# Kernel optimization log

Hardware: AMD Instinct MI355X
Metric: run time of the kernel (lower is better)

## Reference

```python
import jax, jax.numpy as jnp
import numpy as np

HID = 256
NUM_LAYERS = 2


def setup_inputs() -> dict:
    key = jax.random.key(0)
    k0, k1, k2, k3 = jax.random.split(key, 4)
    B, R, C, I = 64, 32, 32, 8
    stdv = 1.0 / np.sqrt(HID)
    inp = jax.random.normal(k0, (B, R, C, I), jnp.float32)
    W_first = jax.random.uniform(k1, (6 * HID, I + 2 * HID), jnp.float32, -stdv, stdv)
    W_other = jax.random.uniform(k2, (NUM_LAYERS - 1, 6 * HID, 4 * HID), jnp.float32, -stdv, stdv)
    Bias = jax.random.uniform(k3, (NUM_LAYERS, 6 * HID), jnp.float32, -stdv, stdv)
    return {"input": inp, "W_first": W_first, "W_other": W_other, "Bias": Bias,
            "batch_size": B, "input_size": I, "flag": 0}


def _run_layer(a, W, b, H):
    # a: [R, B, L, F_in] diagonally-shifted input; W: [6H, F_in+2H]; b: [6H]
    R, Bb, L, _ = a.shape
    C = L - R + 1
    h0 = jnp.zeros((R, Bb, H), a.dtype)

    def step(carry, inputs):
        h_row, h_col = carry
        x_t, t = inputs
        z = jnp.concatenate([h_row, h_col, x_t], axis=-1)        # [R,B,2H+F]
        gate = jnp.einsum('rbf,gf->rbg', z, W)                   # [R,B,6H]
        # torch: bias added only to first B*(t+1) rows, and only when t < R
        mask = ((jnp.arange(R) <= t) & (t < R))[:, None, None]
        gate = jnp.where(mask, gate + b, gate)
        sig = jax.nn.sigmoid(gate[..., :4 * H])
        tnh = jnp.tanh(gate[..., 4 * H:])
        u_r, o_r, u_c, o_c = jnp.split(sig, 4, axis=-1)
        i_r, i_c = jnp.split(tnh, 2, axis=-1)
        h_row = jnp.tanh((1 - u_r) * h_row + u_r * i_r) * o_r
        h_col = jnp.tanh((1 - u_c) * h_col + u_c * i_c) * o_c
        out = jnp.concatenate([h_row, h_col], axis=-1)           # [R,B,2H]
        # row state that would be saved at this step (valid for t >= C-1)
        row_save = jax.lax.dynamic_index_in_dim(
            h_row, jnp.clip(t - (C - 1), 0, R - 1), axis=0, keepdims=False)
        col_save = h_col[R - 1]                                  # saved pre-roll
        h_col = jnp.roll(h_col, 1, axis=0)                       # roll by batch_size == shift slice axis by 1
        return (h_row, h_col), (out, row_save, col_save)

    xs = (jnp.moveaxis(a, 2, 0), jnp.arange(L))
    _, (outs, row_saves, col_saves) = jax.lax.scan(step, (h0, h0), xs)
    a_next = jnp.moveaxis(outs, 0, 2)        # [R, B, L, 2H]
    hidden_row = row_saves[C - 1:]           # [R, B, H]  (steps t >= C-1)
    hidden_col = col_saves[R - 1:]           # [C, B, H]  (steps t >= R-1)
    return a_next, hidden_row, hidden_col


def _forward(input, W_first, W_other, Bias, flag):
    H = Bias.shape[-1] // 6
    num_layers = Bias.shape[0]
    x = jnp.transpose(input, (2, 0, 1, 3)) if flag == 1 else jnp.transpose(input, (1, 0, 2, 3))
    R, Bb, C, I = x.shape
    L = R + C - 1
    # input_transfer[r, :, r:r+C, :] = x[r]  -> pad then roll each slice by r
    xp = jnp.pad(x, ((0, 0), (0, 0), (0, R - 1), (0, 0)))        # [R,B,L,I]
    a = jax.vmap(lambda xr, r: jnp.roll(xr, r, axis=1))(xp, jnp.arange(R))
    rows, cols = [], []
    for layer in range(num_layers):
        W = W_first if layer == 0 else W_other[layer - 1]
        a, hr, hc = _run_layer(a, W, Bias[layer], H)             # dropout=0 / eval: identity
        rows.append(hr)
        cols.append(hc)
    output_all = a.reshape(R * Bb, L, 2 * H)
    hidden_row_all = jnp.transpose(jnp.stack(rows), (2, 0, 1, 3))  # [B, NL, R, H]
    hidden_col_all = jnp.transpose(jnp.stack(cols), (2, 0, 1, 3))  # [B, NL, C, H]
    if flag == 1:
        return output_all, hidden_col_all, hidden_row_all
    return output_all, hidden_row_all, hidden_col_all


def reference(input, W_first, W_other, Bias, batch_size, input_size, flag):
    return _forward(input, W_first, W_other, Bias, flag)
```

## Files before the change

kernel.cpp:

```cpp
#include <hip/hip_runtime.h>

typedef __bf16 bf16x8 __attribute__((ext_vector_type(8)));
typedef float  f32x4  __attribute__((ext_vector_type(4)));

#define Z0S 520
#define Z1S 1032
#define W0P_ELEMS (2 * 8 * 17 * 6 * 512)
#define W1P_ELEMS (2 * 8 * 32 * 6 * 512)
#define XB_ELEMS (2 * 64 * 32 * 512)

__device__ __forceinline__ unsigned short f2bf(float f) {
    unsigned int u = __builtin_bit_cast(unsigned int, f);
    u += 0x7fffu + ((u >> 16) & 1u);
    return (unsigned short)(u >> 16);
}
__device__ __forceinline__ float sigm(float x) {
    x = fminf(30.f, fmaxf(-30.f, x));
    return __fdividef(1.0f, 1.0f + __expf(-x));
}
__device__ __forceinline__ float ftanh(float x) {
    x = fminf(15.f, fmaxf(-15.f, x));
    float e = __expf(2.0f * x);
    return 1.0f - __fdividef(2.0f, e + 1.0f);
}
__device__ __forceinline__ bf16x8 zero8() {
    bf16x8 v;
#pragma unroll
    for (int i = 0; i < 8; ++i) v[i] = (__bf16)0.0f;
    return v;
}
__device__ __forceinline__ void st_f32_wt(float* p, float v) {
    __hip_atomic_store(p, v, __ATOMIC_RELAXED, __HIP_MEMORY_SCOPE_AGENT);
}
__device__ __forceinline__ void st_u16_wt(unsigned short* p, unsigned short v) {
    __hip_atomic_store(p, v, __ATOMIC_RELAXED, __HIP_MEMORY_SCOPE_AGENT);
}

__global__ void convert_w(const float* __restrict__ W0f, const float* __restrict__ W1f,
                          unsigned short* __restrict__ W0p, unsigned short* __restrict__ W1p,
                          int* __restrict__ flags) {
    const int gid = blockIdx.x * blockDim.x + threadIdx.x;
    const int stride = gridDim.x * blockDim.x;
    if (gid < 512) flags[gid] = 0;
    for (int i = gid; i < W0P_ELEMS; i += stride) {
        const int e = i & 7, lane = (i >> 3) & 63;
        const int r = i >> 9;
        const int G = r % 6;  const int r2 = r / 6;
        const int ks = r2 % 17; const int gcg = r2 / 17;
        const int jj = gcg * 16 + (lane & 15);
        const int k = ks * 32 + (lane >> 4) * 8 + e;
        float v = 0.f;
        if (k < 520) v = W0f[(size_t)(G * 256 + jj) * 520 + k];
        W0p[i] = f2bf(v);
    }
    for (int i = gid; i < W1P_ELEMS; i += stride) {
        const int e = i & 7, lane = (i >> 3) & 63;
        const int r = i >> 9;
        const int G = r % 6;  const int r2 = r / 6;
        const int ks = r2 & 31; const int gcg = r2 >> 5;
        const int jj = gcg * 16 + (lane & 15);
        const int k = ks * 32 + (lane >> 4) * 8 + e;
        W1p[i] = f2bf(W1f[(size_t)(G * 256 + jj) * 1024 + k]);
    }
}

__global__ __launch_bounds__(512, 2) void witran_coop(
    const float* __restrict__ inp,
    const unsigned short* __restrict__ W0p,
    const unsigned short* __restrict__ W1p,
    const float* __restrict__ Bias,
    float* __restrict__ out,
    unsigned short* __restrict__ xb0,
    unsigned short* __restrict__ xb1,
    int* __restrict__ flags)
{
    const int bid  = blockIdx.x;
    const int r8   = bid & 7;
    const int s    = r8 >> 1;
    const int b    = (bid >> 3) * 2 + (r8 & 1);
    const int tid  = threadIdx.x;
    const int wave = tid >> 6;
    const int cg   = wave >> 1;
    const int gh   = wave & 1;
    const int lane = tid & 63;
    const int quad = lane >> 4;
    const int l16  = lane & 15;
    const int jl   = cg * 16 + l16;
    const int jj   = s * 64 + jl;
    const int gcg  = jj >> 4;
    const int Gs0 = 2 * gh, Gs1 = 2 * gh + 1, Gs2 = 4 + gh;

    int* f0 = flags;
    int* f1 = flags + 256;
    const int fown = b * 4 + s;

    __shared__ __align__(16) unsigned short z0[32 * Z0S];
    __shared__ __align__(16) unsigned short z1[32 * Z1S];
    __shared__ float rollbuf[32 * 64];

    for (int idx = tid; idx < 32 * Z0S; idx += 512) z0[idx] = 0;
    for (int idx = tid; idx < 32 * Z1S; idx += 512) z1[idx] = 0;
    __syncthreads();
    if (tid < 256) {
        const int m = tid >> 3, i = tid & 7;
        const int c = 0 - m;
        float v = 0.f;
        if (c >= 0 && c < 32) v = inp[((b * 32 + m) * 32 + c) * 8 + i];
        z0[m * Z0S + 512 + i] = f2bf(v);
    }

    float biasr[2][3];
#pragma unroll
    for (int L = 0; L < 2; ++L) {
        biasr[L][0] = Bias[L * 1536 + Gs0 * 256 + jj];
        biasr[L][1] = Bias[L * 1536 + Gs1 * 256 + jj];
        biasr[L][2] = Bias[L * 1536 + Gs2 * 256 + jj];
    }

    float streg[2][2][4];
#pragma unroll
    for (int L = 0; L < 2; ++L)
#pragma unroll
        for (int mh = 0; mh < 2; ++mh)
#pragma unroll
            for (int p = 0; p < 4; ++p) streg[L][mh][p] = 0.f;

    const unsigned short* w0g[3];
    const unsigned short* w1g[3];
    w0g[0] = W0p + (size_t)gcg * (17 * 6 * 512) + Gs0 * 512 + lane * 8;
    w0g[1] = W0p + (size_t)gcg * (17 * 6 * 512) + Gs1 * 512 + lane * 8;
    w0g[2] = W0p + (size_t)gcg * (17 * 6 * 512) + Gs2 * 512 + lane * 8;
    w1g[0] = W1p + (size_t)gcg * (32 * 6 * 512) + Gs0 * 512 + lane * 8;
    w1g[1] = W1p + (size_t)gcg * (32 * 6 * 512) + Gs1 * 512 + lane * 8;
    w1g[2] = W1p + (size_t)gcg * (32 * 6 * 512) + Gs2 * 512 + lane * 8;
    const unsigned short* aB0m[2] = { &z0[l16 * Z0S], &z0[(16 + l16) * Z0S] };
    const unsigned short* aB1m[2] = { &z1[l16 * Z1S], &z1[(16 + l16) * Z1S] };

    __syncthreads();

    const size_t OUT1 = 66060288u;
    const size_t OUT2 = OUT1 + 1048576u;

    const int sr   = tid >> 4;
    const int srem = tid & 15;
    const int sreg = srem >> 3;
    const int sc8  = (srem & 7) * 8;
    const int sr1  = (sr + 1) & 31;

    for (int t = 0; t < 63; ++t) {
        float snew[2][4];
        f32x4 acc[3][2];
        bf16x8 bA[3], bB[3];
#pragma unroll
        for (int i = 0; i < 3; ++i)
#pragma unroll
            for (int mh = 0; mh < 2; ++mh) acc[i][mh] = (f32x4){0.f, 0.f, 0.f, 0.f};
#pragma unroll
        for (int i = 0; i < 3; ++i) bA[i] = *(const bf16x8*)&w0g[i][0];

#pragma unroll 4
        for (int kp = 0; kp < 8; ++kp) {
            bf16x8 a00 = *(const bf16x8*)&aB0m[0][(2 * kp) * 32 + quad * 8];
            bf16x8 a01 = *(const bf16x8*)&aB0m[1][(2 * kp) * 32 + quad * 8];
            bf16x8 a10 = *(const bf16x8*)&aB0m[0][(2 * kp + 1) * 32 + quad * 8];
            bf16x8 a11 = *(const bf16x8*)&aB0m[1][(2 * kp + 1) * 32 + quad * 8];
#pragma unroll
            for (int i = 0; i < 3; ++i) bB[i] = *(const bf16x8*)&w0g[i][(2 * kp + 1) * 3072];
#pragma unroll
            for (int i = 0; i < 3; ++i) {
                acc[i][0] = __builtin_amdgcn_mfma_f32_16x16x32_bf16(a00, bA[i], acc[i][0], 0, 0, 0);
                acc[i][1] = __builtin_amdgcn_mfma_f32_16x16x32_bf16(a01, bA[i], acc[i][1], 0, 0, 0);
            }
#pragma unroll
            for (int i = 0; i < 3; ++i) bA[i] = *(const bf16x8*)&w0g[i][(2 * kp + 2) * 3072];
#pragma unroll
            for (int i = 0; i < 3; ++i) {
                acc[i][0] = __builtin_amdgcn_mfma_f32_16x16x32_bf16(a10, bB[i], acc[i][0], 0, 0, 0);
                acc[i][1] = __builtin_amdgcn_mfma_f32_16x16x32_bf16(a11, bB[i], acc[i][1], 0, 0, 0);
            }
        }
        {
            bf16x8 a0 = zero8(), a1 = zero8();
            if (quad == 0) {
                a0 = *(const bf16x8*)&aB0m[0][512];
                a1 = *(const bf16x8*)&aB0m[1][512];
            }
#pragma unroll
            for (int i = 0; i < 3; ++i) {
                acc[i][0] = __builtin_amdgcn_mfma_f32_16x16x32_bf16(a0, bA[i], acc[i][0], 0, 0, 0);
                acc[i][1] = __builtin_amdgcn_mfma_f32_16x16x32_bf16(a1, bA[i], acc[i][1], 0, 0, 0);
            }
        }

#pragma unroll
        for (int mh = 0; mh < 2; ++mh)
#pragma unroll
            for (int p = 0; p < 4; ++p) {
                const int m = mh * 16 + quad * 4 + p;
                float gu = acc[0][mh][p], go = acc[1][mh][p], gi = acc[2][mh][p];
                if ((t < 32) && (m <= t)) {
                    gu += biasr[0][0]; go += biasr[0][1]; gi += biasr[0][2];
                }
                const float u = sigm(gu), o = sigm(go), ii = ftanh(gi);
                snew[mh][p] = ftanh((1.f - u) * streg[0][mh][p] + u * ii) * o;
            }
        if (gh == 0) {
#pragma unroll
            for (int mh = 0; mh < 2; ++mh)
#pragma unroll
                for (int p = 0; p < 4; ++p) streg[0][mh][p] = snew[mh][p];
        }
        __syncthreads();

#pragma unroll
        for (int mh = 0; mh < 2; ++mh)
#pragma unroll
            for (int p = 0; p < 4; ++p) {
                const int m  = mh * 16 + quad * 4 + p;
                const float f = snew[mh][p];
                const unsigned short hb = f2bf(f);
                const size_t xi = ((size_t)((t & 1) * 64 + b) * 32 + m) * 512;
                if (gh == 0) {
                    z0[m * Z0S + jj] = hb;
                    z1[m * Z1S + 512 + jj] = hb;
                    st_u16_wt(&xb0[xi + jj], hb);
                    if (t >= 31 && m == t - 31)
                        st_f32_wt(&out[OUT1 + ((size_t)(b * 2 + 0) * 32 + (t - 31)) * 256 + jj], f);
                } else {
                    z0[((m + 1) & 31) * Z0S + 256 + jj] = hb;
                    z1[m * Z1S + 768 + jj] = hb;
                    rollbuf[m * 64 + jl] = f;
                    st_u16_wt(&xb0[xi + 256 + jj], hb);
                    if (t >= 31 && m == 31)
                        st_f32_wt(&out[OUT2 + ((size_t)(b * 2 + 0) * 32 + (t - 31)) * 256 + jj], f);
                }
            }
        if (tid < 256 && t + 1 < 63) {
            const int m = tid >> 3, i = tid & 7;
            const int c = t + 1 - m;
            float v = 0.f;
            if (c >= 0 && c < 32) v = inp[((b * 32 + m) * 32 + c) * 8 + i];
            z0[m * Z0S + 512 + i] = f2bf(v);
        }
        __syncthreads();

        if (tid == 0)
            __hip_atomic_store(&f0[fown], t + 1, __ATOMIC_RELEASE, __HIP_MEMORY_SCOPE_AGENT);

        if (gh == 1) {
#pragma unroll
            for (int mh = 0; mh < 2; ++mh)
#pragma unroll
                for (int p = 0; p < 4; ++p) {
                    const int m = mh * 16 + quad * 4 + p;
                    streg[0][mh][p] = rollbuf[((m + 31) & 31) * 64 + jl];
                }
        }

        if (tid == 0) {
#pragma unroll
            for (int j = 1; j < 4; ++j) {
                const int fp = b * 4 + ((s + j) & 3);
                int it = 0;
                while (__hip_atomic_load(&f0[fp], __ATOMIC_RELAXED, __HIP_MEMORY_SCOPE_AGENT) < t + 1) {
                    __builtin_amdgcn_s_sleep(4);
                    if (++it > 4000000) break;
                }
                it = 0;
                while (__hip_atomic_load(&f1[fp], __ATOMIC_RELAXED, __HIP_MEMORY_SCOPE_AGENT) < t) {
                    __builtin_amdgcn_s_sleep(4);
                    if (++it > 4000000) break;
                }
            }
        }
        __syncthreads();

        {
            const unsigned int* x0u = (const unsigned int*)xb0;
            const unsigned int* x1u = (const unsigned int*)xb1;
#pragma unroll
            for (int j = 1; j < 4; ++j) {
                const int q   = (s + j) & 3;
                const int col = q * 64 + sc8;
                union { unsigned int u4[4]; bf16x8 v; } q0, q1;
                const size_t e0 = (((size_t)((t & 1) * 64 + b) * 32 + sr) * 512 + sreg * 256 + col) >> 1;
#pragma unroll
                for (int w = 0; w < 4; ++w)
                    q0.u4[w] = __hip_atomic_load(&x0u[e0 + w], __ATOMIC_RELAXED, __HIP_MEMORY_SCOPE_AGENT);
                *(bf16x8*)&z1[sr * Z1S + 512 + sreg * 256 + col] = q0.v;
                *(bf16x8*)&z0[(sreg ? sr1 : sr) * Z0S + sreg * 256 + col] = q0.v;
                if (t > 0) {
                    const size_t e1 = (((size_t)(((t + 1) & 1) * 64 + b) * 32 + sr) * 512 + sreg * 256 + col) >> 1;
#pragma unroll
                    for (int w = 0; w < 4; ++w)
                        q1.u4[w] = __hip_atomic_load(&x1u[e1 + w], __ATOMIC_RELAXED, __HIP_MEMORY_SCOPE_AGENT);
                    *(bf16x8*)&z1[(sreg ? sr1 : sr) * Z1S + sreg * 256 + col] = q1.v;
                }
            }
        }
        __syncthreads();

#pragma unroll
        for (int i = 0; i < 3; ++i)
#pragma unroll
            for (int mh = 0; mh < 2; ++mh) acc[i][mh] = (f32x4){0.f, 0.f, 0.f, 0.f};
#pragma unroll
        for (int i = 0; i < 3; ++i) bA[i] = *(const bf16x8*)&w1g[i][0];

#pragma unroll 4
        for (int kp = 0; kp < 16; ++kp) {
            bf16x8 a00 = *(const bf16x8*)&aB1m[0][(2 * kp) * 32 + quad * 8];
            bf16x8 a01 = *(const bf16x8*)&aB1m[1][(2 * kp) * 32 + quad * 8];
            bf16x8 a10 = *(const bf16x8*)&aB1m[0][(2 * kp + 1) * 32 + quad * 8];
            bf16x8 a11 = *(const bf16x8*)&aB1m[1][(2 * kp + 1) * 32 + quad * 8];
#pragma unroll
            for (int i = 0; i < 3; ++i) bB[i] = *(const bf16x8*)&w1g[i][(2 * kp + 1) * 3072];
#pragma unroll
            for (int i = 0; i < 3; ++i) {
                acc[i][0] = __builtin_amdgcn_mfma_f32_16x16x32_bf16(a00, bA[i], acc[i][0], 0, 0, 0);
                acc[i][1] = __builtin_amdgcn_mfma_f32_16x16x32_bf16(a01, bA[i], acc[i][1], 0, 0, 0);
            }
            const int kn = (kp < 15) ? (2 * kp + 2) : 31;
#pragma unroll
            for (int i = 0; i < 3; ++i) bA[i] = *(const bf16x8*)&w1g[i][kn * 3072];
#pragma unroll
            for (int i = 0; i < 3; ++i) {
                acc[i][0] = __builtin_amdgcn_mfma_f32_16x16x32_bf16(a10, bB[i], acc[i][0], 0, 0, 0);
                acc[i][1] = __builtin_amdgcn_mfma_f32_16x16x32_bf16(a11, bB[i], acc[i][1], 0, 0, 0);
            }
        }

#pragma unroll
        for (int mh = 0; mh < 2; ++mh)
#pragma unroll
            for (int p = 0; p < 4; ++p) {
                const int m = mh * 16 + quad * 4 + p;
                float gu = acc[0][mh][p], go = acc[1][mh][p], gi = acc[2][mh][p];
                if ((t < 32) && (m <= t)) {
                    gu += biasr[1][0]; go += biasr[1][1]; gi += biasr[1][2];
                }
                const float u = sigm(gu), o = sigm(go), ii = ftanh(gi);
                snew[mh][p] = ftanh((1.f - u) * streg[1][mh][p] + u * ii) * o;
            }
        if (gh == 0) {
#pragma unroll
            for (int mh = 0; mh < 2; ++mh)
#pragma unroll
                for (int p = 0; p < 4; ++p) streg[1][mh][p] = snew[mh][p];
        }
        __syncthreads();

#pragma unroll
        for (int mh = 0; mh < 2; ++mh)
#pragma unroll
            for (int p = 0; p < 4; ++p) {
                const int m  = mh * 16 + quad * 4 + p;
                const float f = snew[mh][p];
                const unsigned short hb = f2bf(f);
                const size_t xi = ((size_t)((t & 1) * 64 + b) * 32 + m) * 512;
                const size_t row = (size_t)(m * 64 + b);
                if (gh == 0) {
                    z1[m * Z1S + jj] = hb;
                    st_u16_wt(&xb1[xi + jj], hb);
                    st_f32_wt(&out[(row * 63 + t) * 512 + jj], f);
                    if (t >= 31 && m == t - 31)
                        st_f32_wt(&out[OUT1 + ((size_t)(b * 2 + 1) * 32 + (t - 31)) * 256 + jj], f);
                } else {
                    z1[((m + 1) & 31) * Z1S + 256 + jj] = hb;
                    rollbuf[m * 64 + jl] = f;
                    st_u16_wt(&xb1[xi + 256 + jj], hb);
                    st_f32_wt(&out[(row * 63 + t) * 512 + 256 + jj], f);
                    if (t >= 31 && m == 31)
                        st_f32_wt(&out[OUT2 + ((size_t)(b * 2 + 1) * 32 + (t - 31)) * 256 + jj], f);
                }
            }
        __syncthreads();

        if (tid == 0)
            __hip_atomic_store(&f1[fown], t + 1, __ATOMIC_RELEASE, __HIP_MEMORY_SCOPE_AGENT);

        if (gh == 1) {
#pragma unroll
            for (int mh = 0; mh < 2; ++mh)
#pragma unroll
                for (int p = 0; p < 4; ++p) {
                    const int m = mh * 16 + quad * 4 + p;
                    streg[1][mh][p] = rollbuf[((m + 31) & 31) * 64 + jl];
                }
        }
    }
}

extern "C" void kernel_launch(void* const* d_in, const int* in_sizes, int n_in,
                              void* d_out, int out_size, void* d_ws, size_t ws_size,
                              hipStream_t stream) {
    (void)in_sizes; (void)n_in; (void)out_size; (void)ws_size;
    const float* inp   = (const float*)d_in[0];
    const float* W0f   = (const float*)d_in[1];
    const float* W1f   = (const float*)d_in[2];
    const float* Biasf = (const float*)d_in[3];
    float* out = (float*)d_out;

    unsigned short* W0p = (unsigned short*)d_ws;
    unsigned short* W1p = W0p + W0P_ELEMS;
    int* flags = (int*)(W1p + W1P_ELEMS);
    unsigned short* xb0 = (unsigned short*)(flags + 512);
    unsigned short* xb1 = xb0 + XB_ELEMS;

    convert_w<<<dim3(512), dim3(256), 0, stream>>>(W0f, W1f, W0p, W1p, flags);
    witran_coop<<<dim3(256), dim3(512), 0, stream>>>(inp, W0p, W1p, Biasf, out,
                                                     xb0, xb1, flags);
}
```

Baseline: 1.933 ms.

## Split the K reduction across wave pairs and double the block size

Blocks grow from 512 to 1024 threads. Each pair of waves now computes half of the K dimension of the gate GEMM for both row halves, then exchanges partial accumulators through a new LDS reduction buffer. Each wave then finishes the activations for only one 16-row half. The cross-block exchange loads for layer 0 and layer 1 are also split between the two thread halves. The aim is to halve the serial MFMA chain per timestep in this latency-bound recurrence, at the cost of an extra LDS round trip and sync, and tighter register and LDS budgets under the new launch bounds.

```diff
diff --git a/kernel.cpp b/kernel.cpp
--- a/kernel.cpp
+++ b/kernel.cpp
@@ -64,7 +64,7 @@
     }
 }
 
-__global__ __launch_bounds__(512, 2) void witran_coop(
+__global__ __launch_bounds__(1024, 4) void witran_coop(
     const float* __restrict__ inp,
     const unsigned short* __restrict__ W0p,
     const unsigned short* __restrict__ W1p,
@@ -80,8 +80,9 @@
     const int b    = (bid >> 3) * 2 + (r8 & 1);
     const int tid  = threadIdx.x;
     const int wave = tid >> 6;
-    const int cg   = wave >> 1;
-    const int gh   = wave & 1;
+    const int cg   = wave >> 2;
+    const int gh   = (wave >> 1) & 1;
+    const int kh   = wave & 1;
     const int lane = tid & 63;
     const int quad = lane >> 4;
     const int l16  = lane & 15;
@@ -97,9 +98,10 @@
     __shared__ __align__(16) unsigned short z0[32 * Z0S];
     __shared__ __align__(16) unsigned short z1[32 * Z1S];
     __shared__ float rollbuf[32 * 64];
-
-    for (int idx = tid; idx < 32 * Z0S; idx += 512) z0[idx] = 0;
-    for (int idx = tid; idx < 32 * Z1S; idx += 512) z1[idx] = 0;
+    __shared__ __align__(16) float red[16 * 3 * 64 * 4];
+
+    for (int idx = tid; idx < 32 * Z0S; idx += 1024) z0[idx] = 0;
+    for (int idx = tid; idx < 32 * Z1S; idx += 1024) z1[idx] = 0;
     __syncthreads();
     if (tid < 256) {
         const int m = tid >> 3, i = tid & 7;
@@ -117,13 +119,11 @@
         biasr[L][2] = Bias[L * 1536 + Gs2 * 256 + jj];
     }
 
-    float streg[2][2][4];
+    float streg[2][4];
 #pragma unroll
     for (int L = 0; L < 2; ++L)
 #pragma unroll
-        for (int mh = 0; mh < 2; ++mh)
-#pragma unroll
-            for (int p = 0; p < 4; ++p) streg[L][mh][p] = 0.f;
+        for (int p = 0; p < 4; ++p) streg[L][p] = 0.f;
 
     const unsigned short* w0g[3];
     const unsigned short* w1g[3];
@@ -136,105 +136,111 @@
     const unsigned short* aB0m[2] = { &z0[l16 * Z0S], &z0[(16 + l16) * Z0S] };
     const unsigned short* aB1m[2] = { &z1[l16 * Z1S], &z1[(16 + l16) * Z1S] };
 
+    float* redw = &red[(wave * 3) * 256 + lane * 4];
+    const float* redr = &red[((wave ^ 1) * 3) * 256 + lane * 4];
+
     __syncthreads();
 
     const size_t OUT1 = 66060288u;
     const size_t OUT2 = OUT1 + 1048576u;
 
-    const int sr   = tid >> 4;
-    const int srem = tid & 15;
+    const int bsel = tid >> 9;
+    const int t9   = tid & 511;
+    const int sr   = t9 >> 4;
+    const int srem = t9 & 15;
     const int sreg = srem >> 3;
     const int sc8  = (srem & 7) * 8;
     const int sr1  = (sr + 1) & 31;
 
     for (int t = 0; t < 63; ++t) {
-        float snew[2][4];
+        float snew[4];
         f32x4 acc[3][2];
         bf16x8 bA[3], bB[3];
+
 #pragma unroll
         for (int i = 0; i < 3; ++i)
 #pragma unroll
             for (int mh = 0; mh < 2; ++mh) acc[i][mh] = (f32x4){0.f, 0.f, 0.f, 0.f};
-#pragma unroll
-        for (int i = 0; i < 3; ++i) bA[i] = *(const bf16x8*)&w0g[i][0];
-
-#pragma unroll 4
-        for (int kp = 0; kp < 8; ++kp) {
-            bf16x8 a00 = *(const bf16x8*)&aB0m[0][(2 * kp) * 32 + quad * 8];
-            bf16x8 a01 = *(const bf16x8*)&aB0m[1][(2 * kp) * 32 + quad * 8];
-            bf16x8 a10 = *(const bf16x8*)&aB0m[0][(2 * kp + 1) * 32 + quad * 8];
-            bf16x8 a11 = *(const bf16x8*)&aB0m[1][(2 * kp + 1) * 32 + quad * 8];
-#pragma unroll
-            for (int i = 0; i < 3; ++i) bB[i] = *(const bf16x8*)&w0g[i][(2 * kp + 1) * 3072];
-#pragma unroll
-            for (int i = 0; i < 3; ++i) {
-                acc[i][0] = __builtin_amdgcn_mfma_f32_16x16x32_bf16(a00, bA[i], acc[i][0], 0, 0, 0);
-                acc[i][1] = __builtin_amdgcn_mfma_f32_16x16x32_bf16(a01, bA[i], acc[i][1], 0, 0, 0);
-            }
-#pragma unroll
-            for (int i = 0; i < 3; ++i) bA[i] = *(const bf16x8*)&w0g[i][(2 * kp + 2) * 3072];
-#pragma unroll
-            for (int i = 0; i < 3; ++i) {
-                acc[i][0] = __builtin_amdgcn_mfma_f32_16x16x32_bf16(a10, bB[i], acc[i][0], 0, 0, 0);
-                acc[i][1] = __builtin_amdgcn_mfma_f32_16x16x32_bf16(a11, bB[i], acc[i][1], 0, 0, 0);
-            }
-        }
         {
-            bf16x8 a0 = zero8(), a1 = zero8();
-            if (quad == 0) {
-                a0 = *(const bf16x8*)&aB0m[0][512];
-                a1 = *(const bf16x8*)&aB0m[1][512];
-            }
-#pragma unroll
-            for (int i = 0; i < 3; ++i) {
-                acc[i][0] = __builtin_amdgcn_mfma_f32_16x16x32_bf16(a0, bA[i], acc[i][0], 0, 0, 0);
-                acc[i][1] = __builtin_amdgcn_mfma_f32_16x16x32_bf16(a1, bA[i], acc[i][1], 0, 0, 0);
-            }
-        }
-
-#pragma unroll
-        for (int mh = 0; mh < 2; ++mh)
-#pragma unroll
-            for (int p = 0; p < 4; ++p) {
-                const int m = mh * 16 + quad * 4 + p;
-                float gu = acc[0][mh][p], go = acc[1][mh][p], gi = acc[2][mh][p];
-                if ((t < 32) && (m <= t)) {
-                    gu += biasr[0][0]; go += biasr[0][1]; gi += biasr[0][2];
-                }
-                const float u = sigm(gu), o = sigm(go), ii = ftanh(gi);
-                snew[mh][p] = ftanh((1.f - u) * streg[0][mh][p] + u * ii) * o;
-            }
+            const int ka = kh ? 9 : 0;
+            const int kb = kh ? 16 : 9;
+#pragma unroll
+            for (int i = 0; i < 3; ++i) bA[i] = *(const bf16x8*)&w0g[i][ka * 3072];
+#pragma unroll 2
+            for (int ks = ka; ks < kb; ++ks) {
+                bf16x8 a0 = *(const bf16x8*)&aB0m[0][ks * 32 + quad * 8];
+                bf16x8 a1 = *(const bf16x8*)&aB0m[1][ks * 32 + quad * 8];
+                const int kn = (ks + 1 < kb) ? ks + 1 : ks;
+#pragma unroll
+                for (int i = 0; i < 3; ++i) bB[i] = *(const bf16x8*)&w0g[i][kn * 3072];
+#pragma unroll
+                for (int i = 0; i < 3; ++i) {
+                    acc[i][0] = __builtin_amdgcn_mfma_f32_16x16x32_bf16(a0, bA[i], acc[i][0], 0, 0, 0);
+                    acc[i][1] = __builtin_amdgcn_mfma_f32_16x16x32_bf16(a1, bA[i], acc[i][1], 0, 0, 0);
+                }
+#pragma unroll
+                for (int i = 0; i < 3; ++i) bA[i] = bB[i];
+            }
+            if (kh) {
+                bf16x8 a0 = zero8(), a1 = zero8();
+                if (quad == 0) {
+                    a0 = *(const bf16x8*)&aB0m[0][512];
+                    a1 = *(const bf16x8*)&aB0m[1][512];
+                }
+#pragma unroll
+                for (int i = 0; i < 3; ++i) bB[i] = *(const bf16x8*)&w0g[i][16 * 3072];
+#pragma unroll
+                for (int i = 0; i < 3; ++i) {
+                    acc[i][0] = __builtin_amdgcn_mfma_f32_16x16x32_bf16(a0, bB[i], acc[i][0], 0, 0, 0);
+                    acc[i][1] = __builtin_amdgcn_mfma_f32_16x16x32_bf16(a1, bB[i], acc[i][1], 0, 0, 0);
+                }
+            }
+        }
+#pragma unroll
+        for (int i = 0; i < 3; ++i) *(f32x4*)&redw[i * 256] = acc[i][1 - kh];
+        __syncthreads();
+#pragma unroll
+        for (int i = 0; i < 3; ++i) {
+            const f32x4 v = *(const f32x4*)&redr[i * 256];
+            acc[i][kh][0] += v[0]; acc[i][kh][1] += v[1];
+            acc[i][kh][2] += v[2]; acc[i][kh][3] += v[3];
+        }
+#pragma unroll
+        for (int p = 0; p < 4; ++p) {
+            const int m = kh * 16 + quad * 4 + p;
+            float gu = acc[0][kh][p], go = acc[1][kh][p], gi = acc[2][kh][p];
+            if ((t < 32) && (m <= t)) {
+                gu += biasr[0][0]; go += biasr[0][1]; gi += biasr[0][2];
+            }
+            const float u = sigm(gu), o = sigm(go), ii = ftanh(gi);
+            snew[p] = ftanh((1.f - u) * streg[0][p] + u * ii) * o;
+        }
         if (gh == 0) {
 #pragma unroll
-            for (int mh = 0; mh < 2; ++mh)
-#pragma unroll
-                for (int p = 0; p < 4; ++p) streg[0][mh][p] = snew[mh][p];
-        }
-        __syncthreads();
-
-#pragma unroll
-        for (int mh = 0; mh < 2; ++mh)
-#pragma unroll
-            for (int p = 0; p < 4; ++p) {
-                const int m  = mh * 16 + quad * 4 + p;
-                const float f = snew[mh][p];
-                const unsigned short hb = f2bf(f);
-                const size_t xi = ((size_t)((t & 1) * 64 + b) * 32 + m) * 512;
-                if (gh == 0) {
-                    z0[m * Z0S + jj] = hb;
-                    z1[m * Z1S + 512 + jj] = hb;
-                    st_u16_wt(&xb0[xi + jj], hb);
-                    if (t >= 31 && m == t - 31)
-                        st_f32_wt(&out[OUT1 + ((size_t)(b * 2 + 0) * 32 + (t - 31)) * 256 + jj], f);
-                } else {
-                    z0[((m + 1) & 31) * Z0S + 256 + jj] = hb;
-                    z1[m * Z1S + 768 + jj] = hb;
-                    rollbuf[m * 64 + jl] = f;
-                    st_u16_wt(&xb0[xi + 256 + jj], hb);
-                    if (t >= 31 && m == 31)
-                        st_f32_wt(&out[OUT2 + ((size_t)(b * 2 + 0) * 32 + (t - 31)) * 256 + jj], f);
-                }
-            }
+            for (int p = 0; p < 4; ++p) streg[0][p] = snew[p];
+        }
+
+#pragma unroll
+        for (int p = 0; p < 4; ++p) {
+            const int m  = kh * 16 + quad * 4 + p;
+            const float f = snew[p];
+            const unsigned short hb = f2bf(f);
+            const size_t xi = ((size_t)((t & 1) * 64 + b) * 32 + m) * 512;
+            if (gh == 0) {
+                z0[m * Z0S + jj] = hb;
+                z1[m * Z1S + 512 + jj] = hb;
+                st_u16_wt(&xb0[xi + jj], hb);
+                if (t >= 31 && m == t - 31)
+                    st_f32_wt(&out[OUT1 + ((size_t)(b * 2 + 0) * 32 + (t - 31)) * 256 + jj], f);
+            } else {
+                z0[((m + 1) & 31) * Z0S + 256 + jj] = hb;
+                z1[m * Z1S + 768 + jj] = hb;
+                rollbuf[m * 64 + jl] = f;
+                st_u16_wt(&xb0[xi + 256 + jj], hb);
+                if (t >= 31 && m == 31)
+                    st_f32_wt(&out[OUT2 + ((size_t)(b * 2 + 0) * 32 + (t - 31)) * 256 + jj], f);
+            }
+        }
         if (tid < 256 && t + 1 < 63) {
             const int m = tid >> 3, i = tid & 7;
             const int c = t + 1 - m;
@@ -249,12 +255,10 @@
 
         if (gh == 1) {
 #pragma unroll
-            for (int mh = 0; mh < 2; ++mh)
-#pragma unroll
-                for (int p = 0; p < 4; ++p) {
-                    const int m = mh * 16 + quad * 4 + p;
-                    streg[0][mh][p] = rollbuf[((m + 31) & 31) * 64 + jl];
-                }
+            for (int p = 0; p < 4; ++p) {
+                const int m = kh * 16 + quad * 4 + p;
+                streg[0][p] = rollbuf[((m + 31) & 31) * 64 + jl];
+            }
         }
 
         if (tid == 0) {
@@ -282,19 +286,20 @@
             for (int j = 1; j < 4; ++j) {
                 const int q   = (s + j) & 3;
                 const int col = q * 64 + sc8;
-                union { unsigned int u4[4]; bf16x8 v; } q0, q1;
-                const size_t e0 = (((size_t)((t & 1) * 64 + b) * 32 + sr) * 512 + sreg * 256 + col) >> 1;
-#pragma unroll
-                for (int w = 0; w < 4; ++w)
-                    q0.u4[w] = __hip_atomic_load(&x0u[e0 + w], __ATOMIC_RELAXED, __HIP_MEMORY_SCOPE_AGENT);
-                *(bf16x8*)&z1[sr * Z1S + 512 + sreg * 256 + col] = q0.v;
-                *(bf16x8*)&z0[(sreg ? sr1 : sr) * Z0S + sreg * 256 + col] = q0.v;
-                if (t > 0) {
+                union { unsigned int u4[4]; bf16x8 v; } qv;
+                if (bsel == 0) {
+                    const size_t e0 = (((size_t)((t & 1) * 64 + b) * 32 + sr) * 512 + sreg * 256 + col) >> 1;
+#pragma unroll
+                    for (int w = 0; w < 4; ++w)
+                        qv.u4[w] = __hip_atomic_load(&x0u[e0 + w], __ATOMIC_RELAXED, __HIP_MEMORY_SCOPE_AGENT);
+                    *(bf16x8*)&z1[sr * Z1S + 512 + sreg * 256 + col] = qv.v;
+                    *(bf16x8*)&z0[(sreg ? sr1 : sr) * Z0S + sreg * 256 + col] = qv.v;
+                } else if (t > 0) {
                     const size_t e1 = (((size_t)(((t + 1) & 1) * 64 + b) * 32 + sr) * 512 + sreg * 256 + col) >> 1;
 #pragma unroll
                     for (int w = 0; w < 4; ++w)
-                        q1.u4[w] = __hip_atomic_load(&x1u[e1 + w], __ATOMIC_RELAXED, __HIP_MEMORY_SCOPE_AGENT);
-                    *(bf16x8*)&z1[(sreg ? sr1 : sr) * Z1S + sreg * 256 + col] = q1.v;
+                        qv.u4[w] = __hip_atomic_load(&x1u[e1 + w], __ATOMIC_RELAXED, __HIP_MEMORY_SCOPE_AGENT);
+                    *(bf16x8*)&z1[(sreg ? sr1 : sr) * Z1S + sreg * 256 + col] = qv.v;
                 }
             }
         }
@@ -304,76 +309,73 @@
         for (int i = 0; i < 3; ++i)
 #pragma unroll
             for (int mh = 0; mh < 2; ++mh) acc[i][mh] = (f32x4){0.f, 0.f, 0.f, 0.f};
-#pragma unroll
-        for (int i = 0; i < 3; ++i) bA[i] = *(const bf16x8*)&w1g[i][0];
-
-#pragma unroll 4
-        for (int kp = 0; kp < 16; ++kp) {
-            bf16x8 a00 = *(const bf16x8*)&aB1m[0][(2 * kp) * 32 + quad * 8];
-            bf16x8 a01 = *(const bf16x8*)&aB1m[1][(2 * kp) * 32 + quad * 8];
-            bf16x8 a10 = *(const bf16x8*)&aB1m[0][(2 * kp + 1) * 32 + quad * 8];
-            bf16x8 a11 = *(const bf16x8*)&aB1m[1][(2 * kp + 1) * 32 + quad * 8];
-#pragma unroll
-            for (int i = 0; i < 3; ++i) bB[i] = *(const bf16x8*)&w1g[i][(2 * kp + 1) * 3072];
-#pragma unroll
-            for (int i = 0; i < 3; ++i) {
-                acc[i][0] = __builtin_amdgcn_mfma_f32_16x16x32_bf16(a00, bA[i], acc[i][0], 0, 0, 0);
-                acc[i][1] = __builtin_amdgcn_mfma_f32_16x16x32_bf16(a01, bA[i], acc[i][1], 0, 0, 0);
-            }
-            const int kn = (kp < 15) ? (2 * kp + 2) : 31;
-#pragma unroll
-            for (int i = 0; i < 3; ++i) bA[i] = *(const bf16x8*)&w1g[i][kn * 3072];
-#pragma unroll
-            for (int i = 0; i < 3; ++i) {
-                acc[i][0] = __builtin_amdgcn_mfma_f32_16x16x32_bf16(a10, bB[i], acc[i][0], 0, 0, 0);
-                acc[i][1] = __builtin_amdgcn_mfma_f32_16x16x32_bf16(a11, bB[i], acc[i][1], 0, 0, 0);
-            }
-        }
-
-#pragma unroll
-        for (int mh = 0; mh < 2; ++mh)
-#pragma unroll
-            for (int p = 0; p < 4; ++p) {
-                const int m = mh * 16 + quad * 4 + p;
-                float gu = acc[0][mh][p], go = acc[1][mh][p], gi = acc[2][mh][p];
-                if ((t < 32) && (m <= t)) {
-                    gu += biasr[1][0]; go += biasr[1][1]; gi += biasr[1][2];
-                }
-                const float u = sigm(gu), o = sigm(go), ii = ftanh(gi);
-                snew[mh][p] = ftanh((1.f - u) * streg[1][mh][p] + u * ii) * o;
-            }
+        {
+            const int ka = kh ? 16 : 0;
+            const int kb = kh ? 32 : 16;
+#pragma unroll
+            for (int i = 0; i < 3; ++i) bA[i] = *(const bf16x8*)&w1g[i][ka * 3072];
+#pragma unroll 2
+            for (int ks = ka; ks < kb; ++ks) {
+                bf16x8 a0 = *(const bf16x8*)&aB1m[0][ks * 32 + quad * 8];
+                bf16x8 a1 = *(const bf16x8*)&aB1m[1][ks * 32 + quad * 8];
+                const int kn = (ks + 1 < kb) ? ks + 1 : ks;
+#pragma unroll
+                for (int i = 0; i < 3; ++i) bB[i] = *(const bf16x8*)&w1g[i][kn * 3072];
+#pragma unroll
+                for (int i = 0; i < 3; ++i) {
+                    acc[i][0] = __builtin_amdgcn_mfma_f32_16x16x32_bf16(a0, bA[i], acc[i][0], 0, 0, 0);
+                    acc[i][1] = __builtin_amdgcn_mfma_f32_16x16x32_bf16(a1, bA[i], acc[i][1], 0, 0, 0);
+                }
+#pragma unroll
+                for (int i = 0; i < 3; ++i) bA[i] = bB[i];
+            }
+        }
+#pragma unroll
+        for (int i = 0; i < 3; ++i) *(f32x4*)&redw[i * 256] = acc[i][1 - kh];
+        __syncthreads();
+#pragma unroll
+        for (int i = 0; i < 3; ++i) {
+            const f32x4 v = *(const f32x4*)&redr[i * 256];
+            acc[i][kh][0] += v[0]; acc[i][kh][1] += v[1];
+            acc[i][kh][2] += v[2]; acc[i][kh][3] += v[3];
+        }
+#pragma unroll
+        for (int p = 0; p < 4; ++p) {
+            const int m = kh * 16 + quad * 4 + p;
+            float gu = acc[0][kh][p], go = acc[1][kh][p], gi = acc[2][kh][p];
+            if ((t < 32) && (m <= t)) {
+                gu += biasr[1][0]; go += biasr[1][1]; gi += biasr[1][2];
+            }
+            const float u = sigm(gu), o = sigm(go), ii = ftanh(gi);
+            snew[p] = ftanh((1.f - u) * streg[1][p] + u * ii) * o;
+        }
         if (gh == 0) {
 #pragma unroll
-            for (int mh = 0; mh < 2; ++mh)
-#pragma unroll
-                for (int p = 0; p < 4; ++p) streg[1][mh][p] = snew[mh][p];
-        }
-        __syncthreads();
-
-#pragma unroll
-        for (int mh = 0; mh < 2; ++mh)
-#pragma unroll
-            for (int p = 0; p < 4; ++p) {
-                const int m  = mh * 16 + quad * 4 + p;
-                const float f = snew[mh][p];
-                const unsigned short hb = f2bf(f);
-                const size_t xi = ((size_t)((t & 1) * 64 + b) * 32 + m) * 512;
-                const size_t row = (size_t)(m * 64 + b);
-                if (gh == 0) {
-                    z1[m * Z1S + jj] = hb;
-                    st_u16_wt(&xb1[xi + jj], hb);
-                    st_f32_wt(&out[(row * 63 + t) * 512 + jj], f);
-                    if (t >= 31 && m == t - 31)
-                        st_f32_wt(&out[OUT1 + ((size_t)(b * 2 + 1) * 32 + (t - 31)) * 256 + jj], f);
-                } else {
-                    z1[((m + 1) & 31) * Z1S + 256 + jj] = hb;
-                    rollbuf[m * 64 + jl] = f;
-                    st_u16_wt(&xb1[xi + 256 + jj], hb);
-                    st_f32_wt(&out[(row * 63 + t) * 512 + 256 + jj], f);
-                    if (t >= 31 && m == 31)
-                        st_f32_wt(&out[OUT2 + ((size_t)(b * 2 + 1) * 32 + (t - 31)) * 256 + jj], f);
-                }
-            }
+            for (int p = 0; p < 4; ++p) streg[1][p] = snew[p];
+        }
+
+#pragma unroll
+        for (int p = 0; p < 4; ++p) {
+            const int m  = kh * 16 + quad * 4 + p;
+            const float f = snew[p];
+            const unsigned short hb = f2bf(f);
+            const size_t xi = ((size_t)((t & 1) * 64 + b) * 32 + m) * 512;
+            const size_t row = (size_t)(m * 64 + b);
+            if (gh == 0) {
+                z1[m * Z1S + jj] = hb;
+                st_u16_wt(&xb1[xi + jj], hb);
+                st_f32_wt(&out[(row * 63 + t) * 512 + jj], f);
+                if (t >= 31 && m == t - 31)
+                    st_f32_wt(&out[OUT1 + ((size_t)(b * 2 + 1) * 32 + (t - 31)) * 256 + jj], f);
+            } else {
+                z1[((m + 1) & 31) * Z1S + 256 + jj] = hb;
+                rollbuf[m * 64 + jl] = f;
+                st_u16_wt(&xb1[xi + 256 + jj], hb);
+                st_f32_wt(&out[(row * 63 + t) * 512 + 256 + jj], f);
+                if (t >= 31 && m == 31)
+                    st_f32_wt(&out[OUT2 + ((size_t)(b * 2 + 1) * 32 + (t - 31)) * 256 + jj], f);
+            }
+        }
         __syncthreads();
 
         if (tid == 0)
@@ -381,12 +383,10 @@
 
         if (gh == 1) {
 #pragma unroll
-            for (int mh = 0; mh < 2; ++mh)
-#pragma unroll
-                for (int p = 0; p < 4; ++p) {
-                    const int m = mh * 16 + quad * 4 + p;
-                    streg[1][mh][p] = rollbuf[((m + 31) & 31) * 64 + jl];
-                }
+            for (int p = 0; p < 4; ++p) {
+                const int m = kh * 16 + quad * 4 + p;
+                streg[1][p] = rollbuf[((m + 31) & 31) * 64 + jl];
+            }
         }
     }
 }
@@ -408,6 +408,6 @@
     unsigned short* xb1 = xb0 + XB_ELEMS;
 
     convert_w<<<dim3(512), dim3(256), 0, stream>>>(W0f, W1f, W0p, W1p, flags);
-    witran_coop<<<dim3(256), dim3(512), 0, stream>>>(inp, W0p, W1p, Biasf, out,
-                                                     xb0, xb1, flags);
-}
+    witran_coop<<<dim3(256), dim3(1024), 0, stream>>>(inp, W0p, W1p, Biasf, out,
+                                                      xb0, xb1, flags);
+}
```

Result: slower. 4.151 ms (+114.7%).
